# Kernel tuning notes

Hardware: AMD Instinct MI355X
Metric: run time of the kernel (lower is better)

## Reference

```python
import jax, jax.numpy as jnp
import numpy as np

B, Q, HID = 2, 1024, 2048
NH, NKV, HD = 32, 8, 64          # num heads, kv heads, head_dim (HID = NH*HD)
GROUPS = NH // NKV
KB_N, TOPK = 512, 100            # kb entries, top_k_kb
KB_MAX_TRAIN = 512               # kb_max_train_triples (kb_length_scaling=True)
ROPE_THETA = 10000.0


def rotate_half(x):
    x1, x2 = jnp.split(x, 2, axis=-1)
    return jnp.concatenate([-x2, x1], axis=-1)


def setup_inputs() -> dict:
    key = jax.random.key(0)
    ks = jax.random.split(key, 10)
    sc = 1.0 / np.sqrt(HID)
    hidden_states = jax.random.normal(ks[0], (B, Q, HID), jnp.float32)
    kb_kvs = jax.random.normal(ks[1], (B, KB_N, HID), jnp.float32)
    Wq = jax.random.normal(ks[2], (HID, NH * HD), jnp.float32) * sc
    Wk = jax.random.normal(ks[3], (HID, NKV * HD), jnp.float32) * sc
    Wv = jax.random.normal(ks[4], (HID, NKV * HD), jnp.float32) * sc
    Wo = jax.random.normal(ks[5], (NH * HD, HID), jnp.float32) * sc
    Wq_new = jax.random.normal(ks[6], (HID, NH * HD), jnp.float32) * sc
    Wkb_k = jax.random.normal(ks[7], (HID, NKV * HD), jnp.float32) * sc
    Wkb_v = jax.random.normal(ks[8], (HID, NKV * HD), jnp.float32) * sc
    # RoPE tables [Q, HD]
    inv_freq = 1.0 / (ROPE_THETA ** (jnp.arange(0, HD, 2, dtype=jnp.float32) / HD))
    t = jnp.arange(Q, dtype=jnp.float32)
    freqs = t[:, None] * inv_freq[None, :]
    emb = jnp.concatenate([freqs, freqs], axis=-1)
    cos, sin = jnp.cos(emb), jnp.sin(emb)
    position_ids = jnp.broadcast_to(jnp.arange(Q), (B, Q))
    # additive causal mask [B,1,Q,Q]
    i = jnp.arange(Q)
    causal = jnp.where(i[None, :] <= i[:, None], 0.0, -1e9).astype(jnp.float32)
    attention_mask = jnp.broadcast_to(causal[None, None], (B, 1, Q, Q))
    return dict(hidden_states=hidden_states, kb_kvs=kb_kvs, Wq=Wq, Wk=Wk, Wv=Wv,
                Wo=Wo, Wq_new=Wq_new, Wkb_k=Wkb_k, Wkb_v=Wkb_v, cos=cos, sin=sin,
                attention_mask=attention_mask, position_ids=position_ids)


def attention_fwd(hidden_states, kb_kvs, Wq, Wk, Wv, Wo, Wq_new, Wkb_k, Wkb_v,
                  cos, sin, attention_mask, position_ids):
    b, q_len, _ = hidden_states.shape
    q = (hidden_states @ Wq).reshape(b, q_len, NH, HD).transpose(0, 2, 1, 3)
    k = (hidden_states @ Wk).reshape(b, q_len, NKV, HD).transpose(0, 2, 1, 3)
    v = (hidden_states @ Wv).reshape(b, q_len, NKV, HD).transpose(0, 2, 1, 3)
    # RoPE
    c = cos[position_ids][:, None]  # [b,1,q,hd]
    s = sin[position_ids][:, None]
    q = q * c + rotate_half(q) * s
    k = k * c + rotate_half(k) * s
    # repeat_kv (GQA expansion)
    k = jnp.repeat(k, GROUPS, axis=1)
    v = jnp.repeat(v, GROUPS, axis=1)
    # KB branch (layer_idx=0, kb_layer_index=0 -> slice is full hidden dim)
    kb_k = (kb_kvs @ Wkb_k).reshape(b, KB_N, NKV, HD).transpose(0, 2, 1, 3)
    kb_v = (kb_kvs @ Wkb_v).reshape(b, KB_N, NKV, HD).transpose(0, 2, 1, 3)
    kb_k = jnp.repeat(kb_k, GROUPS, axis=1)
    kb_v = jnp.repeat(kb_v, GROUPS, axis=1)
    kb_q = (hidden_states @ Wq_new).reshape(b, q_len, NH, HD).transpose(0, 2, 1, 3)
    scale = 1.0 / jnp.sqrt(jnp.float32(HD))
    aw_kb = jnp.einsum('bhqd,bhkd->bhqk', kb_q, kb_k) * scale  # [b,nh,q,KB_N]
    # top-k KB entry selection (scores summed over heads and query positions)
    sel_scores = aw_kb.sum(axis=(1, 2))                        # [b,KB_N]
    _, top_idx = jax.lax.top_k(sel_scores, TOPK)               # [b,TOPK]
    kb_v = jnp.take_along_axis(kb_v, top_idx[:, None, :, None], axis=2)
    aw_kb = jnp.take_along_axis(aw_kb, top_idx[:, None, None, :], axis=3)
    # kb length scaling: log(max_train_triples) - log(current kb len)
    aw_kb = aw_kb + (jnp.log(jnp.float32(KB_MAX_TRAIN)) - jnp.log(jnp.float32(TOPK)))
    aw_p = jnp.einsum('bhqd,bhkd->bhqk', q, k) * scale + attention_mask
    aw = jax.nn.softmax(jnp.concatenate([aw_kb, aw_p], axis=-1).astype(jnp.float32), axis=-1)
    aw = aw.astype(q.dtype)
    cv = jnp.concatenate([kb_v, v], axis=2)                    # [b,nh,TOPK+q,hd]
    out = jnp.einsum('bhqk,bhkd->bhqd', aw, cv)
    out = out.transpose(0, 2, 1, 3).reshape(b, q_len, NH * HD)
    return out @ Wo


def reference(hidden_states, kb_kvs, Wq, Wk, Wv, Wo, Wq_new, Wkb_k, Wkb_v,
              cos, sin, attention_mask, position_ids):
    return attention_fwd(hidden_states, kb_kvs, Wq, Wk, Wv, Wo, Wq_new, Wkb_k,
                         Wkb_v, cos, sin, attention_mask, position_ids)
```

## Files before the change

### kernel.cpp

```cpp
#include <hip/hip_runtime.h>

typedef unsigned short u16;
typedef unsigned int   u32;
typedef __bf16 bf16_t;
typedef bf16_t bf16x8 __attribute__((ext_vector_type(8)));
typedef float  floatx4 __attribute__((ext_vector_type(4)));

#define B_    2
#define QS    1024
#define HID_  2048
#define NH_   32
#define NKV_  8
#define HD_   64
#define KBN_  512
#define TOPK_ 100
#define FS    5120

__device__ __forceinline__ float b2f(u16 u) {
  union { u32 i; float f; } x; x.i = ((u32)u) << 16; return x.f;
}
__device__ __forceinline__ u16 f2b(float f) {
  union { float f; u32 i; } x; x.f = f;
  u32 r = x.i + 0x7fffu + ((x.i >> 16) & 1u);
  return (u16)(r >> 16);
}
__device__ __forceinline__ void async16(const u16* g, u16* l) {
  __builtin_amdgcn_global_load_lds(
      (const __attribute__((address_space(1))) unsigned int*)g,
      (__attribute__((address_space(3))) unsigned int*)l, 16, 0, 0);
}

__global__ __launch_bounds__(256)
void tc7_k(const float* __restrict__ Wq, const float* __restrict__ Wk,
           const float* __restrict__ Wv, const float* __restrict__ Wqn,
           const float* __restrict__ Wkbk, const float* __restrict__ Wkbv,
           const float* __restrict__ Wo, u16* __restrict__ WT,
           u16* __restrict__ WTkb, u16* __restrict__ WTo,
           const float* __restrict__ hs, const float* __restrict__ kb,
           u16* __restrict__ hsb, u16* __restrict__ kbb) {
  int id = blockIdx.x, t = threadIdx.x;
  if (id >= 16384) {
    const float* x; u16* y; int j;
    if (id < 20480) { x = hs; y = hsb; j = (id - 16384) * 256 + t; }
    else            { x = kb; y = kbb; j = (id - 20480) * 256 + t; }
    float4 v = ((const float4*)x)[j];
    ((uint2*)y)[j] = make_uint2((u32)f2b(v.x) | ((u32)f2b(v.y) << 16),
                                (u32)f2b(v.z) | ((u32)f2b(v.w) << 16));
    return;
  }
  const float* W; u16* D; int N, bx, by;
  if (id < 4096)       { W = Wq;   D = WT;                        N = 2048; int l = id;         bx = l & 63; by = l >> 6; }
  else if (id < 5120)  { W = Wk;   D = WT + (size_t)2048 * 2048;  N = 512;  int l = id - 4096;  bx = l & 15; by = l >> 4; }
  else if (id < 6144)  { W = Wv;   D = WT + (size_t)2560 * 2048;  N = 512;  int l = id - 5120;  bx = l & 15; by = l >> 4; }
  else if (id < 10240) { W = Wqn;  D = WT + (size_t)3072 * 2048;  N = 2048; int l = id - 6144;  bx = l & 63; by = l >> 6; }
  else if (id < 11264) { W = Wkbk; D = WTkb;                      N = 512;  int l = id - 10240; bx = l & 15; by = l >> 4; }
  else if (id < 12288) { W = Wkbv; D = WTkb + (size_t)512 * 2048; N = 512;  int l = id - 11264; bx = l & 15; by = l >> 4; }
  else                 { W = Wo;   D = WTo;                       N = 2048; int l = id - 12288; bx = l & 63; by = l >> 6; }
  const int K = 2048;
  __shared__ float tile[32][33];
  int n0 = bx * 32, k0 = by * 32;
  int tx = t & 31, ty = t >> 5;
#pragma unroll
  for (int i = 0; i < 32; i += 8)
    tile[ty + i][tx] = W[(size_t)(k0 + ty + i) * N + n0 + tx];
  __syncthreads();
#pragma unroll
  for (int i = 0; i < 32; i += 8)
    D[(size_t)(n0 + ty + i) * K + k0 + tx] = f2b(tile[tx][ty + i]);
}

__global__ __launch_bounds__(512, 2)
void gemm256j(const u16* __restrict__ A0, const u16* __restrict__ B0,
              u16* __restrict__ C0, const u16* __restrict__ A1,
              const u16* __restrict__ B1, u16* __restrict__ C1, int K) {
  __shared__ __align__(16) u16 sm[65536];
  const int tid = threadIdx.x, lane = tid & 63, w = tid >> 6;
  const int wr = w >> 2, wc = w & 3;
  int orig = blockIdx.x;
  int swz = (orig & 7) * 22 + (orig >> 3);
  const u16 *A, *BT; u16* C; int CS, bx, by;
  if (swz < 160) { A = A0; BT = B0; C = C0; CS = FS;   bx = swz % 20; by = swz / 20; }
  else { int t2 = swz - 160; A = A1; BT = B1; C = C1; CS = 1024; bx = t2 & 3; by = t2 >> 2; }
  int m0 = by << 8, n0 = bx << 8;
  const int NT = K >> 6;

  int lr = lane >> 2;
  int colsw = ((lane & 3) * 8) ^ ((lane & 32) ? 16 : 0);
  const u16* gA[2][2]; const u16* gB[2][2];
  int lA[2][2];
#pragma unroll
  for (int h = 0; h < 2; ++h)
#pragma unroll
    for (int j = 0; j < 2; ++j) {
      int ij = 2 * w + j, kk = ij >> 3, rb = (ij & 7) * 16;
      gA[h][j] = A + (size_t)(m0 + h * 128 + rb + lr) * K + kk * 32 + colsw;
      gB[h][j] = BT + (size_t)(n0 + h * 128 + rb + lr) * K + kk * 32 + colsw;
      lA[h][j] = kk * 8192 + (h * 128 + rb) * 32;
    }
  int fsw = ((lane >> 4) * 8) ^ ((lane & 8) ? 16 : 0);
  int aoff = (wr * 128 + (lane & 15)) * 32 + fsw;
  int boff = 16384 + (wc * 64 + (lane & 15)) * 32 + fsw;

  floatx4 acc[8][4];
#pragma unroll
  for (int i = 0; i < 8; ++i)
#pragma unroll
    for (int j = 0; j < 4; ++j) acc[i][j] = (floatx4){0.f, 0.f, 0.f, 0.f};
  bf16x8 a[4][2], b[4][2];

#define STG_(g, l, u) async16((g) + (size_t)(u) * 64, &sm[(((u) & 1) << 15) + (l)])
#define BAR_ do { asm volatile("" ::: "memory"); __builtin_amdgcn_s_barrier(); \
                  asm volatile("" ::: "memory"); } while (0)
#define LG0_ do { asm volatile("s_waitcnt lgkmcnt(0)" ::: "memory"); \
                  __builtin_amdgcn_sched_barrier(0); } while (0)

  STG_(gA[0][0], lA[0][0], 0); STG_(gA[0][1], lA[0][1], 0);
  STG_(gA[1][0], lA[1][0], 0); STG_(gA[1][1], lA[1][1], 0);
  STG_(gB[0][0], lA[0][0] + 16384, 0); STG_(gB[0][1], lA[0][1] + 16384, 0);
  STG_(gB[1][0], lA[1][0] + 16384, 0); STG_(gB[1][1], lA[1][1] + 16384, 0);
  if (NT > 1) {
    STG_(gB[0][0], lA[0][0] + 16384, 1); STG_(gB[0][1], lA[0][1] + 16384, 1);
    STG_(gA[0][0], lA[0][0], 1); STG_(gA[0][1], lA[0][1], 1);
    asm volatile("s_waitcnt vmcnt(4)" ::: "memory");
  } else {
    asm volatile("s_waitcnt vmcnt(0)" ::: "memory");
  }
  BAR_;

  for (int u = 0; u < NT; ++u) {
    const int cb = (u & 1) << 15;
#pragma unroll
    for (int kk = 0; kk < 2; ++kk) {
#pragma unroll
      for (int mi = 0; mi < 4; ++mi)
        a[mi][kk] = *(const bf16x8*)&sm[cb + kk * 8192 + aoff + mi * 512];
#pragma unroll
      for (int ni = 0; ni < 2; ++ni)
        b[ni][kk] = *(const bf16x8*)&sm[cb + kk * 8192 + boff + ni * 512];
    }
    if (u + 1 < NT) { STG_(gA[1][0], lA[1][0], u + 1); STG_(gA[1][1], lA[1][1], u + 1); }
    BAR_; LG0_;
    __builtin_amdgcn_s_setprio(1);
#pragma unroll
    for (int mi = 0; mi < 4; ++mi)
#pragma unroll
      for (int ni = 0; ni < 2; ++ni)
#pragma unroll
        for (int kk = 0; kk < 2; ++kk)
          acc[mi][ni] = __builtin_amdgcn_mfma_f32_16x16x32_bf16(
              a[mi][kk], b[ni][kk], acc[mi][ni], 0, 0, 0);
    __builtin_amdgcn_s_setprio(0);
    BAR_;
#pragma unroll
    for (int kk = 0; kk < 2; ++kk)
#pragma unroll
      for (int ni = 0; ni < 2; ++ni)
        b[2 + ni][kk] = *(const bf16x8*)&sm[cb + kk * 8192 + boff + (2 + ni) * 512];
    if (u + 1 < NT) { STG_(gB[1][0], lA[1][0] + 16384, u + 1);
                      STG_(gB[1][1], lA[1][1] + 16384, u + 1); }
    BAR_; LG0_;
    __builtin_amdgcn_s_setprio(1);
#pragma unroll
    for (int mi = 0; mi < 4; ++mi)
#pragma unroll
      for (int ni = 0; ni < 2; ++ni)
#pragma unroll
        for (int kk = 0; kk < 2; ++kk)
          acc[mi][2 + ni] = __builtin_amdgcn_mfma_f32_16x16x32_bf16(
              a[mi][kk], b[2 + ni][kk], acc[mi][2 + ni], 0, 0, 0);
    __builtin_amdgcn_s_setprio(0);
    BAR_;
#pragma unroll
    for (int kk = 0; kk < 2; ++kk)
#pragma unroll
      for (int mi = 0; mi < 4; ++mi)
        a[mi][kk] = *(const bf16x8*)&sm[cb + kk * 8192 + aoff + 2048 + mi * 512];
    if (u + 2 < NT) { STG_(gB[0][0], lA[0][0] + 16384, u + 2);
                      STG_(gB[0][1], lA[0][1] + 16384, u + 2); }
    BAR_; LG0_;
    __builtin_amdgcn_s_setprio(1);
#pragma unroll
    for (int mi = 0; mi < 4; ++mi)
#pragma unroll
      for (int ni = 0; ni < 2; ++ni)
#pragma unroll
        for (int kk = 0; kk < 2; ++kk)
          acc[4 + mi][2 + ni] = __builtin_amdgcn_mfma_f32_16x16x32_bf16(
              a[mi][kk], b[2 + ni][kk], acc[4 + mi][2 + ni], 0, 0, 0);
    __builtin_amdgcn_s_setprio(0);
    BAR_;
    if (u + 2 < NT) {
      STG_(gA[0][0], lA[0][0], u + 2); STG_(gA[0][1], lA[0][1], u + 2);
      asm volatile("s_waitcnt vmcnt(4)" ::: "memory");
    } else {
      asm volatile("s_waitcnt vmcnt(0)" ::: "memory");
    }
    BAR_;
    __builtin_amdgcn_s_setprio(1);
#pragma unroll
    for (int mi = 0; mi < 4; ++mi)
#pragma unroll
      for (int ni = 0; ni < 2; ++ni)
#pragma unroll
        for (int kk = 0; kk < 2; ++kk)
          acc[4 + mi][ni] = __builtin_amdgcn_mfma_f32_16x16x32_bf16(
              a[mi][kk], b[ni][kk], acc[4 + mi][ni], 0, 0, 0);
    __builtin_amdgcn_s_setprio(0);
    BAR_;
  }
#undef STG_
#undef BAR_
#undef LG0_
  int quad = lane >> 4, col = lane & 15;
#pragma unroll
  for (int mi = 0; mi < 8; ++mi)
#pragma unroll
    for (int ni = 0; ni < 4; ++ni)
#pragma unroll
      for (int rr = 0; rr < 4; ++rr)
        C[(size_t)(m0 + wr * 128 + mi * 16 + quad * 4 + rr) * CS +
          n0 + wc * 64 + ni * 16 + col] = f2b(acc[mi][ni][rr]);
}

__global__ __launch_bounds__(512, 2)
void gemm256s(const u16* __restrict__ A, const u16* __restrict__ BT,
              float* __restrict__ P, int N, int LDK, int Kl, int ntiles) {
  __shared__ __align__(16) u16 sm[65536];
  const int tid = threadIdx.x, lane = tid & 63, w = tid >> 6;
  const int wr = w >> 2, wc = w & 3;
  const int nbx = N >> 8;
  int nwg = gridDim.x, orig = blockIdx.x, swz = orig;
  if ((nwg & 7) == 0) swz = (orig & 7) * (nwg >> 3) + (orig >> 3);
  int tile = swz % ntiles, slice = swz / ntiles;
  int bx = tile % nbx, by = tile / nbx;
  int m0 = by << 8, n0 = bx << 8;
  const int NT = Kl >> 6;
  const u16* As = A + (size_t)slice * Kl;
  const u16* Bs = BT + (size_t)slice * Kl;

  int lr = lane >> 2;
  int colsw = ((lane & 3) * 8) ^ ((lane & 32) ? 16 : 0);
  const u16* gA[2][2]; const u16* gB[2][2];
  int lA[2][2];
#pragma unroll
  for (int h = 0; h < 2; ++h)
#pragma unroll
    for (int j = 0; j < 2; ++j) {
      int ij = 2 * w + j, kk = ij >> 3, rb = (ij & 7) * 16;
      gA[h][j] = As + (size_t)(m0 + h * 128 + rb + lr) * LDK + kk * 32 + colsw;
      gB[h][j] = Bs + (size_t)(n0 + h * 128 + rb + lr) * LDK + kk * 32 + colsw;
      lA[h][j] = kk * 8192 + (h * 128 + rb) * 32;
    }
  int fsw = ((lane >> 4) * 8) ^ ((lane & 8) ? 16 : 0);
  int aoff = (wr * 128 + (lane & 15)) * 32 + fsw;
  int boff = 16384 + (wc * 64 + (lane & 15)) * 32 + fsw;

  floatx4 acc[8][4];
#pragma unroll
  for (int i = 0; i < 8; ++i)
#pragma unroll
    for (int j = 0; j < 4; ++j) acc[i][j] = (floatx4){0.f, 0.f, 0.f, 0.f};
  bf16x8 a[4][2], b[4][2];

#define STG_(g, l, u) async16((g) + (size_t)(u) * 64, &sm[(((u) & 1) << 15) + (l)])
#define BAR_ do { asm volatile("" ::: "memory"); __builtin_amdgcn_s_barrier(); \
                  asm volatile("" ::: "memory"); } while (0)
#define LG0_ do { asm volatile("s_waitcnt lgkmcnt(0)" ::: "memory"); \
                  __builtin_amdgcn_sched_barrier(0); } while (0)

  STG_(gA[0][0], lA[0][0], 0); STG_(gA[0][1], lA[0][1], 0);
  STG_(gA[1][0], lA[1][0], 0); STG_(gA[1][1], lA[1][1], 0);
  STG_(gB[0][0], lA[0][0] + 16384, 0); STG_(gB[0][1], lA[0][1] + 16384, 0);
  STG_(gB[1][0], lA[1][0] + 16384, 0); STG_(gB[1][1], lA[1][1] + 16384, 0);
  if (NT > 1) {
    STG_(gB[0][0], lA[0][0] + 16384, 1); STG_(gB[0][1], lA[0][1] + 16384, 1);
    STG_(gA[0][0], lA[0][0], 1); STG_(gA[0][1], lA[0][1], 1);
    asm volatile("s_waitcnt vmcnt(4)" ::: "memory");
  } else {
    asm volatile("s_waitcnt vmcnt(0)" ::: "memory");
  }
  BAR_;

  for (int u = 0; u < NT; ++u) {
    const int cb = (u & 1) << 15;
#pragma unroll
    for (int kk = 0; kk < 2; ++kk) {
#pragma unroll
      for (int mi = 0; mi < 4; ++mi)
        a[mi][kk] = *(const bf16x8*)&sm[cb + kk * 8192 + aoff + mi * 512];
#pragma unroll
      for (int ni = 0; ni < 2; ++ni)
        b[ni][kk] = *(const bf16x8*)&sm[cb + kk * 8192 + boff + ni * 512];
    }
    if (u + 1 < NT) { STG_(gA[1][0], lA[1][0], u + 1); STG_(gA[1][1], lA[1][1], u + 1); }
    BAR_; LG0_;
    __builtin_amdgcn_s_setprio(1);
#pragma unroll
    for (int mi = 0; mi < 4; ++mi)
#pragma unroll
      for (int ni = 0; ni < 2; ++ni)
#pragma unroll
        for (int kk = 0; kk < 2; ++kk)
          acc[mi][ni] = __builtin_amdgcn_mfma_f32_16x16x32_bf16(
              a[mi][kk], b[ni][kk], acc[mi][ni], 0, 0, 0);
    __builtin_amdgcn_s_setprio(0);
    BAR_;
#pragma unroll
    for (int kk = 0; kk < 2; ++kk)
#pragma unroll
      for (int ni = 0; ni < 2; ++ni)
        b[2 + ni][kk] = *(const bf16x8*)&sm[cb + kk * 8192 + boff + (2 + ni) * 512];
    if (u + 1 < NT) { STG_(gB[1][0], lA[1][0] + 16384, u + 1);
                      STG_(gB[1][1], lA[1][1] + 16384, u + 1); }
    BAR_; LG0_;
    __builtin_amdgcn_s_setprio(1);
#pragma unroll
    for (int mi = 0; mi < 4; ++mi)
#pragma unroll
      for (int ni = 0; ni < 2; ++ni)
#pragma unroll
        for (int kk = 0; kk < 2; ++kk)
          acc[mi][2 + ni] = __builtin_amdgcn_mfma_f32_16x16x32_bf16(
              a[mi][kk], b[2 + ni][kk], acc[mi][2 + ni], 0, 0, 0);
    __builtin_amdgcn_s_setprio(0);
    BAR_;
#pragma unroll
    for (int kk = 0; kk < 2; ++kk)
#pragma unroll
      for (int mi = 0; mi < 4; ++mi)
        a[mi][kk] = *(const bf16x8*)&sm[cb + kk * 8192 + aoff + 2048 + mi * 512];
    if (u + 2 < NT) { STG_(gB[0][0], lA[0][0] + 16384, u + 2);
                      STG_(gB[0][1], lA[0][1] + 16384, u + 2); }
    BAR_; LG0_;
    __builtin_amdgcn_s_setprio(1);
#pragma unroll
    for (int mi = 0; mi < 4; ++mi)
#pragma unroll
      for (int ni = 0; ni < 2; ++ni)
#pragma unroll
        for (int kk = 0; kk < 2; ++kk)
          acc[4 + mi][2 + ni] = __builtin_amdgcn_mfma_f32_16x16x32_bf16(
              a[mi][kk], b[2 + ni][kk], acc[4 + mi][2 + ni], 0, 0, 0);
    __builtin_amdgcn_s_setprio(0);
    BAR_;
    if (u + 2 < NT) {
      STG_(gA[0][0], lA[0][0], u + 2); STG_(gA[0][1], lA[0][1], u + 2);
      asm volatile("s_waitcnt vmcnt(4)" ::: "memory");
    } else {
      asm volatile("s_waitcnt vmcnt(0)" ::: "memory");
    }
    BAR_;
    __builtin_amdgcn_s_setprio(1);
#pragma unroll
    for (int mi = 0; mi < 4; ++mi)
#pragma unroll
      for (int ni = 0; ni < 2; ++ni)
#pragma unroll
        for (int kk = 0; kk < 2; ++kk)
          acc[4 + mi][ni] = __builtin_amdgcn_mfma_f32_16x16x32_bf16(
              a[mi][kk], b[ni][kk], acc[4 + mi][ni], 0, 0, 0);
    __builtin_amdgcn_s_setprio(0);
    BAR_;
  }
#undef STG_
#undef BAR_
#undef LG0_
  int quad = lane >> 4, col = lane & 15;
  float* Pp = P + (size_t)slice * ((size_t)ntiles << 16);
#pragma unroll
  for (int mi = 0; mi < 8; ++mi)
#pragma unroll
    for (int ni = 0; ni < 4; ++ni)
#pragma unroll
      for (int rr = 0; rr < 4; ++rr)
        Pp[(size_t)(m0 + wr * 128 + mi * 16 + quad * 4 + rr) * N +
           n0 + wc * 64 + ni * 16 + col] = acc[mi][ni][rr];
}

__global__ __launch_bounds__(256)
void redp_k(const float* __restrict__ P, float* __restrict__ out, int nslice, int len4) {
  int i = blockIdx.x * 256 + threadIdx.x;
  if (i >= len4) return;
  float4 a = ((const float4*)P)[i];
  for (int s = 1; s < nslice; ++s) {
    float4 b = ((const float4*)P)[(size_t)s * len4 + i];
    a.x += b.x; a.y += b.y; a.z += b.z; a.w += b.w;
  }
  ((float4*)out)[i] = a;
}

__global__ __launch_bounds__(256)
void rv_k(u16* __restrict__ fused, const float* __restrict__ ct,
          const float* __restrict__ st, const int* __restrict__ pid,
          u16* __restrict__ vt) {
  int bid = blockIdx.x, t = threadIdx.x;
  if (bid < 10240) {
    int gid = bid * 256 + t;
    const int nq = B_ * QS * NH_ * 32;
    u16* x; int nh, g2;
    if (gid < nq) { x = fused;        nh = NH_;  g2 = gid; }
    else          { x = fused + 2048; nh = NKV_; g2 = gid - nq; }
    int per_row = nh * 32;
    int row = g2 / per_row;
    int rem = g2 - row * per_row;
    int h = rem >> 5, d = rem & 31;
    int pos = pid[row];
    float c = ct[pos * 64 + d];
    float s = st[pos * 64 + d];
    size_t base = (size_t)row * FS + h * 64 + d;
    float x0 = b2f(x[base]), x1 = b2f(x[base + 32]);
    x[base]      = f2b(x0 * c - x1 * s);
    x[base + 32] = f2b(x1 * c + x0 * s);
    return;
  }
  int l = bid - 10240;
  int kt = l & 15, bg = l >> 4;
  int b = bg >> 3, g = bg & 7;
  __shared__ u16 tile[64][72];
  {
    int kk = t >> 2, dc = (t & 3) * 16;
    const u16* src = fused + (size_t)(b * QS + kt * 64 + kk) * FS + 2560 + g * 64 + dc;
    *(uint4*)&tile[kk][dc]     = *(const uint4*)src;
    *(uint4*)&tile[kk][dc + 8] = *(const uint4*)(src + 8);
  }
  __syncthreads();
  {
    int d = t >> 2, kc = t & 3;
    __align__(16) u16 tmp[16];
#pragma unroll
    for (int i = 0; i < 16; ++i) tmp[i] = tile[kc * 16 + i][d];
    u16* dst = vt + ((size_t)bg * 64 + d) * 1024 + kt * 64 + kc * 16;
    *(uint4*)dst       = *(uint4*)&tmp[0];
    *(uint4*)(dst + 8) = *(uint4*)&tmp[8];
  }
}

__global__ __launch_bounds__(256)
void hssum_part_k(const float* __restrict__ hs, double* __restrict__ part) {
  int qc = blockIdx.x, b = blockIdx.y, t = threadIdx.x;
  double a[8] = {0, 0, 0, 0, 0, 0, 0, 0};
  for (int qq = 0; qq < 16; ++qq) {
    const float* row = hs + (size_t)(b * QS + qc * 16 + qq) * HID_;
#pragma unroll
    for (int m = 0; m < 8; ++m) a[m] += (double)row[m * 256 + t];
  }
#pragma unroll
  for (int m = 0; m < 8; ++m)
    part[(size_t)qc * (B_ * HID_) + b * HID_ + m * 256 + t] = a[m];
}

__global__ __launch_bounds__(512)
void selS2_k(const double* __restrict__ partH, const float* __restrict__ Wqn,
             double* __restrict__ part) {
  int chunk = blockIdx.x, b = blockIdx.y, j = threadIdx.x;
  int g = j >> 6, d = j & 63;
  int c0 = chunk * 16;
  __shared__ double tmp[64][16];
  __shared__ double hsl[16];
  {
    int e = j;
    int ch = e >> 4, cc = e & 15;
    tmp[ch][cc]      = partH[(size_t)ch * (B_ * HID_) + b * HID_ + c0 + cc];
    tmp[ch + 32][cc] = partH[(size_t)(ch + 32) * (B_ * HID_) + b * HID_ + c0 + cc];
  }
  __syncthreads();
  if (j < 16) {
    double a = 0.0;
    for (int ch = 0; ch < 64; ++ch) a += tmp[ch][j];
    hsl[j] = a;
  }
  __syncthreads();
  double acc = 0.0;
  for (int cc = 0; cc < 16; ++cc) {
    int c = c0 + cc;
    const float* w = Wqn + (size_t)c * HID_ + g * 256 + d;
    acc += hsl[cc] *
           ((double)w[0] + (double)w[64] + (double)w[128] + (double)w[192]);
  }
  part[(size_t)chunk * (B_ * 512) + b * 512 + j] = acc;
}

__global__ __launch_bounds__(256)
void selU2_k(const double* __restrict__ partS, const float* __restrict__ Wkbk,
             double* __restrict__ part) {
  int jc = blockIdx.x;
  int b = blockIdx.y >> 3;
  int c = (blockIdx.y & 7) * 256 + threadIdx.x;
  int t = threadIdx.x;
  __shared__ double buf[32][128];
  __shared__ double Sl[128];
  double a = 0.0;
  if (t < 128) { }
  for (int pass = 0; pass < 4; ++pass) {
    int chb = pass * 32;
#pragma unroll
    for (int e = t; e < 4096; e += 256) {
      int ch = e >> 7, jj = e & 127;
      buf[ch][jj] = partS[(size_t)(chb + ch) * (B_ * 512) + b * 512 + jc * 128 + jj];
    }
    __syncthreads();
    if (t < 128) {
      for (int ch = 0; ch < 32; ++ch) a += buf[ch][t];
    }
    __syncthreads();
  }
  if (t < 128) Sl[t] = a;
  __syncthreads();
  const float* row = Wkbk + (size_t)c * 512 + jc * 128;
  double acc = 0.0;
  for (int j = 0; j < 128; j += 4) {
    float4 wv = *(const float4*)(row + j);
    acc += Sl[j] * (double)wv.x + Sl[j + 1] * (double)wv.y +
           Sl[j + 2] * (double)wv.z + Sl[j + 3] * (double)wv.w;
  }
  part[(size_t)jc * (B_ * HID_) + b * HID_ + c] = acc;
}

__global__ __launch_bounds__(256)
void self2_k(const double* __restrict__ partU, const float* __restrict__ kbin,
             double* __restrict__ part) {
  int n = blockIdx.x * 256 + threadIdx.x;
  int cc = blockIdx.y, b = blockIdx.z;
  int t = threadIdx.x;
  __shared__ double ul[256];
  {
    size_t ui = (size_t)b * HID_ + cc * 256 + t;
    double a = partU[ui];
    a += partU[(size_t)(B_ * HID_) + ui];
    a += partU[2 * (size_t)(B_ * HID_) + ui];
    a += partU[3 * (size_t)(B_ * HID_) + ui];
    ul[t] = a;
  }
  __syncthreads();
  const float* row = kbin + (size_t)(b * KBN_ + n) * HID_ + cc * 256;
  double acc = 0.0;
  for (int c = 0; c < 256; c += 4) {
    float4 kv = *(const float4*)(row + c);
    acc += ul[c] * (double)kv.x + ul[c + 1] * (double)kv.y +
           ul[c + 2] * (double)kv.z + ul[c + 3] * (double)kv.w;
  }
  part[(size_t)cc * (B_ * KBN_) + b * KBN_ + n] = acc;
}

__global__ __launch_bounds__(512)
void topk_rank_k(const double* __restrict__ partSel, int* __restrict__ idx) {
  int b = blockIdx.x, i = threadIdx.x;
  __shared__ float v[KBN_];
  double a = 0.0;
#pragma unroll
  for (int c = 0; c < 8; ++c) a += partSel[(size_t)c * (B_ * KBN_) + b * KBN_ + i];
  float vi = (float)a;
  v[i] = vi;
  __syncthreads();
  int rank = 0;
#pragma unroll 8
  for (int j = 0; j < KBN_; ++j) {
    float vj = v[j];
    rank += (vj > vi || (vj == vi && j < i)) ? 1 : 0;
  }
  if (rank < TOPK_) idx[b * TOPK_ + rank] = i;
}

__global__ __launch_bounds__(256)
void kbgather_k(const u16* __restrict__ kbf, const int* __restrict__ topidx,
                u16* __restrict__ kbt) {
  int bg = blockIdx.x; int b = bg >> 3, g = bg & 7;
  int t = threadIdx.x;
  int d = t >> 2, s0 = (t & 3) * 32;
  __align__(16) u16 tmp[32];
#pragma unroll
  for (int i = 0; i < 32; ++i) {
    int slot = s0 + i;
    int n = topidx[b * TOPK_ + (slot < TOPK_ ? slot : TOPK_ - 1)];
    tmp[i] = kbf[(size_t)(b * KBN_ + n) * 1024 + 512 + g * 64 + d];
  }
  u16* dst = kbt + ((size_t)bg * 64 + d) * 128 + s0;
#pragma unroll
  for (int i = 0; i < 32; i += 8) *(uint4*)(dst + i) = *(uint4*)&tmp[i];
}

__global__ __launch_bounds__(256)
void attn_mfma_k(const u16* __restrict__ fused, const u16* __restrict__ kbf,
                 const u16* __restrict__ vt, const u16* __restrict__ kbt,
                 const int* __restrict__ topidx, u16* __restrict__ ctx) {
  int bid = blockIdx.x;
  int raw = bid >> 6;
  int hb = bid & 63;
  int h = hb & 31, b = hb >> 5;
  int pg = raw >> 2, pp = raw & 3;
  int pbase = (pg >> 1) * 4 + pp;
  int qt = (pg & 1) ? (15 - pbase) : pbase;
  int g = h >> 2;
  int t = threadIdx.x, lane = t & 63, w = t >> 6;
  int quad = lane >> 4, col = lane & 15;
  __shared__ __align__(16) u16 ks[64 * 72];
  __shared__ __align__(16) u16 vst[64 * 64];
  __shared__ __align__(16) u16 ps[4][16 * 72];
  const float LOGADJ = 1.6331544f;
  int q0 = qt * 64;

  int qrow_frag = q0 + w * 16 + col;
  bf16x8 aKB[2], aC[2];
#pragma unroll
  for (int kstep = 0; kstep < 2; ++kstep) {
    const u16* p1 = fused + (size_t)(b * QS + qrow_frag) * FS + 3072 + h * 64 + kstep * 32 + quad * 8;
    const u16* p2 = fused + (size_t)(b * QS + qrow_frag) * FS + 0    + h * 64 + kstep * 32 + quad * 8;
    uint4 x1 = *(const uint4*)p1, x2 = *(const uint4*)p2;
    const u16* u1 = (const u16*)&x1; const u16* u2 = (const u16*)&x2;
#pragma unroll
    for (int i = 0; i < 8; ++i) {
      aKB[kstep][i] = (bf16_t)(0.125f * b2f(u1[i]));
      aC[kstep][i]  = (bf16_t)(0.125f * b2f(u2[i]));
    }
  }

  float mrow[4] = {-1e30f, -1e30f, -1e30f, -1e30f};
  float lrow[4] = {0.f, 0.f, 0.f, 0.f};
  floatx4 acc[4];
#pragma unroll
  for (int nb = 0; nb < 4; ++nb) acc[nb] = (floatx4){0.f, 0.f, 0.f, 0.f};

  int sj = t >> 2, sdc = (t & 3) * 16, sc4 = t & 3;
  uint4 kr0, kr1, vr0, vr1;

#define LOADTILE(TT) do {                                                      \
    int _t = (TT);                                                             \
    const u16 *_src, *_vsrc;                                                   \
    if (_t < 2) {                                                              \
      int _slot = _t * 64 + sj;                                                \
      int _n = topidx[b * TOPK_ + (_slot < TOPK_ ? _slot : TOPK_ - 1)];        \
      _src = kbf + (size_t)(b * KBN_ + _n) * 1024 + g * 64 + sdc;              \
      _vsrc = kbt + ((size_t)(b * 8 + g) * 64 + sj) * 128 + _t * 64 + sc4 * 16;\
    } else {                                                                   \
      int _key = (_t - 2) * 64 + sj;                                           \
      _src = fused + (size_t)(b * QS + _key) * FS + 2048 + g * 64 + sdc;       \
      _vsrc = vt + ((size_t)(b * 8 + g) * 64 + sj) * 1024 + (_t - 2) * 64 + sc4 * 16; \
    }                                                                          \
    kr0 = *(const uint4*)_src;  kr1 = *(const uint4*)(_src + 8);               \
    vr0 = *(const uint4*)_vsrc; vr1 = *(const uint4*)(_vsrc + 8);              \
  } while (0)

  int ntiles = 2 + (q0 >> 6) + 1;
  LOADTILE(0);
  for (int tile = 0; tile < ntiles; ++tile) {
    __syncthreads();
    *(uint4*)&ks[sj * 72 + sdc]     = kr0;
    *(uint4*)&ks[sj * 72 + sdc + 8] = kr1;
    {
      int sw = sj & 7;
      *(uint4*)&vst[sj * 64 + ((2 * sc4)     ^ sw) * 8] = vr0;
      *(uint4*)&vst[sj * 64 + ((2 * sc4 + 1) ^ sw) * 8] = vr1;
    }
    if (tile + 1 < ntiles) LOADTILE(tile + 1);
    __syncthreads();

    bf16x8 aq0 = (tile < 2) ? aKB[0] : aC[0];
    bf16x8 aq1 = (tile < 2) ? aKB[1] : aC[1];
    floatx4 s[4];
#pragma unroll
    for (int nb = 0; nb < 4; ++nb) {
      s[nb] = (floatx4){0.f, 0.f, 0.f, 0.f};
      bf16x8 b0 = *(bf16x8*)&ks[(nb * 16 + col) * 72 + quad * 8];
      bf16x8 b1 = *(bf16x8*)&ks[(nb * 16 + col) * 72 + 32 + quad * 8];
      s[nb] = __builtin_amdgcn_mfma_f32_16x16x32_bf16(aq0, b0, s[nb], 0, 0, 0);
      s[nb] = __builtin_amdgcn_mfma_f32_16x16x32_bf16(aq1, b1, s[nb], 0, 0, 0);
    }
    if (tile < 2) {
      if (tile == 0) {
#pragma unroll
        for (int nb = 0; nb < 4; ++nb)
#pragma unroll
          for (int rr = 0; rr < 4; ++rr) s[nb][rr] += LOGADJ;
      } else {
#pragma unroll
        for (int nb = 0; nb < 4; ++nb) {
          bool dead = (64 + nb * 16 + col) >= TOPK_;
#pragma unroll
          for (int rr = 0; rr < 4; ++rr)
            s[nb][rr] = dead ? -1e30f : (s[nb][rr] + LOGADJ);
        }
      }
    } else if (tile == ntiles - 1) {
      int kbase = (tile - 2) * 64;
#pragma unroll
      for (int nb = 0; nb < 4; ++nb) {
        int key = kbase + nb * 16 + col;
#pragma unroll
        for (int rr = 0; rr < 4; ++rr) {
          int qrow = q0 + w * 16 + quad * 4 + rr;
          if (key > qrow) s[nb][rr] = -1e30f;
        }
      }
    }
    float tm[4];
#pragma unroll
    for (int rr = 0; rr < 4; ++rr)
      tm[rr] = fmaxf(fmaxf(s[0][rr], s[1][rr]), fmaxf(s[2][rr], s[3][rr]));
#pragma unroll
    for (int off = 1; off < 16; off <<= 1)
#pragma unroll
      for (int rr = 0; rr < 4; ++rr)
        tm[rr] = fmaxf(tm[rr], __shfl_xor(tm[rr], off));
    float alpha[4], rs[4];
#pragma unroll
    for (int rr = 0; rr < 4; ++rr) {
      float mn = fmaxf(mrow[rr], tm[rr]);
      alpha[rr] = __expf(mrow[rr] - mn);
      mrow[rr] = mn;
      rs[rr] = 0.f;
    }
#pragma unroll
    for (int nb = 0; nb < 4; ++nb)
#pragma unroll
      for (int rr = 0; rr < 4; ++rr) {
        float ev = __expf(s[nb][rr] - mrow[rr]);
        rs[rr] += ev;
        ps[w][(quad * 4 + rr) * 72 + nb * 16 + col] = f2b(ev);
      }
#pragma unroll
    for (int off = 1; off < 16; off <<= 1)
#pragma unroll
      for (int rr = 0; rr < 4; ++rr)
        rs[rr] += __shfl_xor(rs[rr], off);
#pragma unroll
    for (int rr = 0; rr < 4; ++rr) lrow[rr] = lrow[rr] * alpha[rr] + rs[rr];
#pragma unroll
    for (int nb = 0; nb < 4; ++nb)
#pragma unroll
      for (int rr = 0; rr < 4; ++rr) acc[nb][rr] *= alpha[rr];

    bf16x8 pa0 = *(bf16x8*)&ps[w][col * 72 + quad * 8];
    bf16x8 pa1 = *(bf16x8*)&ps[w][col * 72 + 32 + quad * 8];
#pragma unroll
    for (int nb = 0; nb < 4; ++nb) {
      int d = nb * 16 + col;
      int sw = (d & 7) << 3;
      bf16x8 vb0 = *(bf16x8*)&vst[d * 64 + ((quad * 8) ^ sw)];
      bf16x8 vb1 = *(bf16x8*)&vst[d * 64 + ((32 + quad * 8) ^ sw)];
      acc[nb] = __builtin_amdgcn_mfma_f32_16x16x32_bf16(pa0, vb0, acc[nb], 0, 0, 0);
      acc[nb] = __builtin_amdgcn_mfma_f32_16x16x32_bf16(pa1, vb1, acc[nb], 0, 0, 0);
    }
  }
#undef LOADTILE
#pragma unroll
  for (int rr = 0; rr < 4; ++rr) {
    float inv = 1.f / lrow[rr];
    int qrow = q0 + w * 16 + quad * 4 + rr;
    size_t base = (size_t)(b * QS + qrow) * HID_ + h * 64;
#pragma unroll
    for (int nb = 0; nb < 4; ++nb)
      ctx[base + nb * 16 + col] = f2b(acc[nb][rr] * inv);
  }
}

extern "C" void kernel_launch(void* const* d_in, const int* in_sizes, int n_in,
                              void* d_out, int out_size, void* d_ws, size_t ws_size,
                              hipStream_t stream) {
  (void)in_sizes; (void)n_in; (void)out_size; (void)ws_size;
  const float* hs_f = (const float*)d_in[0];
  const float* kb_f = (const float*)d_in[1];
  const float* Wq   = (const float*)d_in[2];
  const float* Wk   = (const float*)d_in[3];
  const float* Wv   = (const float*)d_in[4];
  const float* Wo   = (const float*)d_in[5];
  const float* Wqn  = (const float*)d_in[6];
  const float* Wkbk = (const float*)d_in[7];
  const float* Wkbv = (const float*)d_in[8];
  const float* cosT = (const float*)d_in[9];
  const float* sinT = (const float*)d_in[10];
  const int*   pid  = (const int*)d_in[12];
  float* out = (float*)d_out;

  char* p = (char*)d_ws;
  u16* WT    = (u16*)p; p += (size_t)FS * 2048 * 2;
  u16* WTkb  = (u16*)p; p += (size_t)1024 * 2048 * 2;
  u16* WTo   = (u16*)p; p += (size_t)2048 * 2048 * 2;
  u16* fused = (u16*)p; p += (size_t)B_ * QS * FS * 2;
  u16* hs_b  = (u16*)p; p += (size_t)B_ * QS * HID_ * 2;
  u16* kb_b  = (u16*)p; p += (size_t)B_ * KBN_ * HID_ * 2;
  u16* kbf   = (u16*)p; p += (size_t)B_ * KBN_ * 1024 * 2;
  int*    idx_ws   = (int*)p;    p += (size_t)B_ * TOPK_ * 4 + 4;
  double* partH    = (double*)p; p += (size_t)64 * B_ * HID_ * 8;
  double* partS    = (double*)p; p += (size_t)128 * B_ * 512 * 8;
  double* partU    = (double*)p; p += (size_t)4 * B_ * HID_ * 8;
  double* partSel  = (double*)p; p += (size_t)8 * B_ * KBN_ * 8;
  float*  partKG   = (float*)p;  p += (size_t)4 * 2048 * 2048 * 4;
  u16* ctx_ws = hs_b;
  u16* v_t    = kb_b;
  u16* kb_t   = kb_b + (size_t)B_ * 8 * 64 * 1024;

  dim3 blk(256);
  tc7_k<<<dim3(22528), blk, 0, stream>>>(Wq, Wk, Wv, Wqn, Wkbk, Wkbv, Wo,
                                         WT, WTkb, WTo, hs_f, kb_f, hs_b, kb_b);
  gemm256j<<<dim3(176), dim3(512), 0, stream>>>(hs_b, WT, fused, kb_b, WTkb, kbf, 2048);
  rv_k<<<dim3(10496), blk, 0, stream>>>(fused, cosT, sinT, pid, v_t);
  hssum_part_k<<<dim3(64, B_), blk, 0, stream>>>(hs_f, partH);
  selS2_k<<<dim3(128, B_), dim3(512), 0, stream>>>(partH, Wqn, partS);
  selU2_k<<<dim3(4, B_ * 8), blk, 0, stream>>>(partS, Wkbk, partU);
  self2_k<<<dim3(2, 8, B_), blk, 0, stream>>>(partU, kb_f, partSel);
  topk_rank_k<<<dim3(B_), dim3(512), 0, stream>>>(partSel, idx_ws);
  kbgather_k<<<dim3(B_ * 8), blk, 0, stream>>>(kbf, idx_ws, kb_t);
  attn_mfma_k<<<dim3(16 * NH_ * B_), blk, 0, stream>>>(fused, kbf, v_t, kb_t, idx_ws, ctx_ws);
  gemm256s<<<dim3(64 * 4), dim3(512), 0, stream>>>(ctx_ws, WTo, partKG, 2048, 2048, 512, 64);
  redp_k<<<dim3((2048 * 2048 / 4 + 255) / 256), blk, 0, stream>>>(
      partKG, out, 4, 2048 * 2048 / 4);
}
```

Before: 368.4 us.

## Fold selection-score kernels into existing launches and use atomic split-K output

The hs-sum, selS and selU kernels become extra blocks appended to the transpose, projection GEMM and RoPE/V-transpose kernels, which removes three launches and lets that small work run alongside the big kernels. The split-K output GEMM now adds its slices straight into a zeroed output with float atomics instead of writing a 64MB partial buffer and running a separate reduction kernel. In exchange it adds a memset, atomic contention on every output element, and a summation order that is no longer deterministic. The side-work blocks also share the GEMM's large shared-memory allocation, which can affect occupancy for those blocks.

```diff
diff --git a/kernel.cpp b/kernel.cpp
--- a/kernel.cpp
+++ b/kernel.cpp
@@ -37,8 +37,23 @@
            const float* __restrict__ Wo, u16* __restrict__ WT,
            u16* __restrict__ WTkb, u16* __restrict__ WTo,
            const float* __restrict__ hs, const float* __restrict__ kb,
-           u16* __restrict__ hsb, u16* __restrict__ kbb) {
+           u16* __restrict__ hsb, u16* __restrict__ kbb,
+           double* __restrict__ partH) {
   int id = blockIdx.x, t = threadIdx.x;
+  if (id >= 22528) {
+    int l = id - 22528;
+    int qc = l & 63, b = l >> 6;
+    double a[8] = {0, 0, 0, 0, 0, 0, 0, 0};
+    for (int qq = 0; qq < 16; ++qq) {
+      const float* row = hs + (size_t)(b * QS + qc * 16 + qq) * HID_;
+#pragma unroll
+      for (int m = 0; m < 8; ++m) a[m] += (double)row[m * 256 + t];
+    }
+#pragma unroll
+    for (int m = 0; m < 8; ++m)
+      partH[(size_t)qc * (B_ * HID_) + b * HID_ + m * 256 + t] = a[m];
+    return;
+  }
   if (id >= 16384) {
     const float* x; u16* y; int j;
     if (id < 20480) { x = hs; y = hsb; j = (id - 16384) * 256 + t; }
@@ -72,11 +87,42 @@
 __global__ __launch_bounds__(512, 2)
 void gemm256j(const u16* __restrict__ A0, const u16* __restrict__ B0,
               u16* __restrict__ C0, const u16* __restrict__ A1,
-              const u16* __restrict__ B1, u16* __restrict__ C1, int K) {
+              const u16* __restrict__ B1, u16* __restrict__ C1, int K,
+              const double* __restrict__ partH, const float* __restrict__ Wqn,
+              double* __restrict__ partS) {
   __shared__ __align__(16) u16 sm[65536];
   const int tid = threadIdx.x, lane = tid & 63, w = tid >> 6;
+  int orig = blockIdx.x;
+  if (orig >= 176) {
+    int l = orig - 176;
+    int chunk = l & 127, b = l >> 7, j = tid;
+    double* tmpd = (double*)sm;
+    double* hsl  = tmpd + 1024;
+    int g = j >> 6, d = j & 63;
+    int c0 = chunk * 16;
+    {
+      int ch = j >> 4, cc = j & 15;
+      tmpd[ch * 16 + cc]        = partH[(size_t)ch * (B_ * HID_) + b * HID_ + c0 + cc];
+      tmpd[(ch + 32) * 16 + cc] = partH[(size_t)(ch + 32) * (B_ * HID_) + b * HID_ + c0 + cc];
+    }
+    __syncthreads();
+    if (j < 16) {
+      double a = 0.0;
+      for (int ch = 0; ch < 64; ++ch) a += tmpd[ch * 16 + j];
+      hsl[j] = a;
+    }
+    __syncthreads();
+    double acc = 0.0;
+    for (int cc = 0; cc < 16; ++cc) {
+      int c = c0 + cc;
+      const float* wq = Wqn + (size_t)c * HID_ + g * 256 + d;
+      acc += hsl[cc] *
+             ((double)wq[0] + (double)wq[64] + (double)wq[128] + (double)wq[192]);
+    }
+    partS[(size_t)chunk * (B_ * 512) + b * 512 + j] = acc;
+    return;
+  }
   const int wr = w >> 2, wc = w & 3;
-  int orig = blockIdx.x;
   int swz = (orig & 7) * 22 + (orig >> 3);
   const u16 *A, *BT; u16* C; int CS, bx, by;
   if (swz < 160) { A = A0; BT = B0; C = C0; CS = FS;   bx = swz % 20; by = swz / 20; }
@@ -224,7 +270,7 @@
 
 __global__ __launch_bounds__(512, 2)
 void gemm256s(const u16* __restrict__ A, const u16* __restrict__ BT,
-              float* __restrict__ P, int N, int LDK, int Kl, int ntiles) {
+              float* __restrict__ Out, int N, int LDK, int Kl, int ntiles) {
   __shared__ __align__(16) u16 sm[65536];
   const int tid = threadIdx.x, lane = tid & 63, w = tid >> 6;
   const int wr = w >> 2, wc = w & 3;
@@ -366,33 +412,22 @@
 #undef BAR_
 #undef LG0_
   int quad = lane >> 4, col = lane & 15;
-  float* Pp = P + (size_t)slice * ((size_t)ntiles << 16);
 #pragma unroll
   for (int mi = 0; mi < 8; ++mi)
 #pragma unroll
     for (int ni = 0; ni < 4; ++ni)
 #pragma unroll
       for (int rr = 0; rr < 4; ++rr)
-        Pp[(size_t)(m0 + wr * 128 + mi * 16 + quad * 4 + rr) * N +
-           n0 + wc * 64 + ni * 16 + col] = acc[mi][ni][rr];
-}
-
-__global__ __launch_bounds__(256)
-void redp_k(const float* __restrict__ P, float* __restrict__ out, int nslice, int len4) {
-  int i = blockIdx.x * 256 + threadIdx.x;
-  if (i >= len4) return;
-  float4 a = ((const float4*)P)[i];
-  for (int s = 1; s < nslice; ++s) {
-    float4 b = ((const float4*)P)[(size_t)s * len4 + i];
-    a.x += b.x; a.y += b.y; a.z += b.z; a.w += b.w;
-  }
-  ((float4*)out)[i] = a;
+        unsafeAtomicAdd(&Out[(size_t)(m0 + wr * 128 + mi * 16 + quad * 4 + rr) * N +
+                             n0 + wc * 64 + ni * 16 + col], acc[mi][ni][rr]);
 }
 
 __global__ __launch_bounds__(256)
 void rv_k(u16* __restrict__ fused, const float* __restrict__ ct,
           const float* __restrict__ st, const int* __restrict__ pid,
-          u16* __restrict__ vt) {
+          u16* __restrict__ vt, const double* __restrict__ partS,
+          const float* __restrict__ Wkbk, double* __restrict__ partU) {
+  __shared__ __align__(16) char rsm[33792];
   int bid = blockIdx.x, t = threadIdx.x;
   if (bid < 10240) {
     int gid = bid * 256 + t;
@@ -413,107 +448,59 @@
     x[base + 32] = f2b(x1 * c + x0 * s);
     return;
   }
+  if (bid >= 10496) {
+    int l = bid - 10496;
+    int jc = l & 3, yy = l >> 2;
+    int b = yy >> 3;
+    int c = (yy & 7) * 256 + t;
+    double* buf = (double*)rsm;
+    double* Sl  = (double*)(rsm + 32768);
+    double a = 0.0;
+    for (int pass = 0; pass < 4; ++pass) {
+      int chb = pass * 32;
+#pragma unroll
+      for (int e = t; e < 4096; e += 256) {
+        int ch = e >> 7, jj = e & 127;
+        buf[ch * 128 + jj] = partS[(size_t)(chb + ch) * (B_ * 512) + b * 512 + jc * 128 + jj];
+      }
+      __syncthreads();
+      if (t < 128) {
+        for (int ch = 0; ch < 32; ++ch) a += buf[ch * 128 + t];
+      }
+      __syncthreads();
+    }
+    if (t < 128) Sl[t] = a;
+    __syncthreads();
+    const float* row = Wkbk + (size_t)c * 512 + jc * 128;
+    double acc = 0.0;
+    for (int j = 0; j < 128; j += 4) {
+      float4 wv = *(const float4*)(row + j);
+      acc += Sl[j] * (double)wv.x + Sl[j + 1] * (double)wv.y +
+             Sl[j + 2] * (double)wv.z + Sl[j + 3] * (double)wv.w;
+    }
+    partU[(size_t)jc * (B_ * HID_) + b * HID_ + c] = acc;
+    return;
+  }
   int l = bid - 10240;
   int kt = l & 15, bg = l >> 4;
   int b = bg >> 3, g = bg & 7;
-  __shared__ u16 tile[64][72];
+  u16* tile = (u16*)rsm;
   {
     int kk = t >> 2, dc = (t & 3) * 16;
     const u16* src = fused + (size_t)(b * QS + kt * 64 + kk) * FS + 2560 + g * 64 + dc;
-    *(uint4*)&tile[kk][dc]     = *(const uint4*)src;
-    *(uint4*)&tile[kk][dc + 8] = *(const uint4*)(src + 8);
+    *(uint4*)&tile[kk * 72 + dc]     = *(const uint4*)src;
+    *(uint4*)&tile[kk * 72 + dc + 8] = *(const uint4*)(src + 8);
   }
   __syncthreads();
   {
     int d = t >> 2, kc = t & 3;
     __align__(16) u16 tmp[16];
 #pragma unroll
-    for (int i = 0; i < 16; ++i) tmp[i] = tile[kc * 16 + i][d];
+    for (int i = 0; i < 16; ++i) tmp[i] = tile[(kc * 16 + i) * 72 + d];
     u16* dst = vt + ((size_t)bg * 64 + d) * 1024 + kt * 64 + kc * 16;
     *(uint4*)dst       = *(uint4*)&tmp[0];
     *(uint4*)(dst + 8) = *(uint4*)&tmp[8];
   }
-}
-
-__global__ __launch_bounds__(256)
-void hssum_part_k(const float* __restrict__ hs, double* __restrict__ part) {
-  int qc = blockIdx.x, b = blockIdx.y, t = threadIdx.x;
-  double a[8] = {0, 0, 0, 0, 0, 0, 0, 0};
-  for (int qq = 0; qq < 16; ++qq) {
-    const float* row = hs + (size_t)(b * QS + qc * 16 + qq) * HID_;
-#pragma unroll
-    for (int m = 0; m < 8; ++m) a[m] += (double)row[m * 256 + t];
-  }
-#pragma unroll
-  for (int m = 0; m < 8; ++m)
-    part[(size_t)qc * (B_ * HID_) + b * HID_ + m * 256 + t] = a[m];
-}
-
-__global__ __launch_bounds__(512)
-void selS2_k(const double* __restrict__ partH, const float* __restrict__ Wqn,
-             double* __restrict__ part) {
-  int chunk = blockIdx.x, b = blockIdx.y, j = threadIdx.x;
-  int g = j >> 6, d = j & 63;
-  int c0 = chunk * 16;
-  __shared__ double tmp[64][16];
-  __shared__ double hsl[16];
-  {
-    int e = j;
-    int ch = e >> 4, cc = e & 15;
-    tmp[ch][cc]      = partH[(size_t)ch * (B_ * HID_) + b * HID_ + c0 + cc];
-    tmp[ch + 32][cc] = partH[(size_t)(ch + 32) * (B_ * HID_) + b * HID_ + c0 + cc];
-  }
-  __syncthreads();
-  if (j < 16) {
-    double a = 0.0;
-    for (int ch = 0; ch < 64; ++ch) a += tmp[ch][j];
-    hsl[j] = a;
-  }
-  __syncthreads();
-  double acc = 0.0;
-  for (int cc = 0; cc < 16; ++cc) {
-    int c = c0 + cc;
-    const float* w = Wqn + (size_t)c * HID_ + g * 256 + d;
-    acc += hsl[cc] *
-           ((double)w[0] + (double)w[64] + (double)w[128] + (double)w[192]);
-  }
-  part[(size_t)chunk * (B_ * 512) + b * 512 + j] = acc;
-}
-
-__global__ __launch_bounds__(256)
-void selU2_k(const double* __restrict__ partS, const float* __restrict__ Wkbk,
-             double* __restrict__ part) {
-  int jc = blockIdx.x;
-  int b = blockIdx.y >> 3;
-  int c = (blockIdx.y & 7) * 256 + threadIdx.x;
-  int t = threadIdx.x;
-  __shared__ double buf[32][128];
-  __shared__ double Sl[128];
-  double a = 0.0;
-  if (t < 128) { }
-  for (int pass = 0; pass < 4; ++pass) {
-    int chb = pass * 32;
-#pragma unroll
-    for (int e = t; e < 4096; e += 256) {
-      int ch = e >> 7, jj = e & 127;
-      buf[ch][jj] = partS[(size_t)(chb + ch) * (B_ * 512) + b * 512 + jc * 128 + jj];
-    }
-    __syncthreads();
-    if (t < 128) {
-      for (int ch = 0; ch < 32; ++ch) a += buf[ch][t];
-    }
-    __syncthreads();
-  }
-  if (t < 128) Sl[t] = a;
-  __syncthreads();
-  const float* row = Wkbk + (size_t)c * 512 + jc * 128;
-  double acc = 0.0;
-  for (int j = 0; j < 128; j += 4) {
-    float4 wv = *(const float4*)(row + j);
-    acc += Sl[j] * (double)wv.x + Sl[j + 1] * (double)wv.y +
-           Sl[j + 2] * (double)wv.z + Sl[j + 3] * (double)wv.w;
-  }
-  part[(size_t)jc * (B_ * HID_) + b * HID_ + c] = acc;
 }
 
 __global__ __launch_bounds__(256)
@@ -784,24 +771,21 @@
   double* partS    = (double*)p; p += (size_t)128 * B_ * 512 * 8;
   double* partU    = (double*)p; p += (size_t)4 * B_ * HID_ * 8;
   double* partSel  = (double*)p; p += (size_t)8 * B_ * KBN_ * 8;
-  float*  partKG   = (float*)p;  p += (size_t)4 * 2048 * 2048 * 4;
   u16* ctx_ws = hs_b;
   u16* v_t    = kb_b;
   u16* kb_t   = kb_b + (size_t)B_ * 8 * 64 * 1024;
 
   dim3 blk(256);
-  tc7_k<<<dim3(22528), blk, 0, stream>>>(Wq, Wk, Wv, Wqn, Wkbk, Wkbv, Wo,
-                                         WT, WTkb, WTo, hs_f, kb_f, hs_b, kb_b);
-  gemm256j<<<dim3(176), dim3(512), 0, stream>>>(hs_b, WT, fused, kb_b, WTkb, kbf, 2048);
-  rv_k<<<dim3(10496), blk, 0, stream>>>(fused, cosT, sinT, pid, v_t);
-  hssum_part_k<<<dim3(64, B_), blk, 0, stream>>>(hs_f, partH);
-  selS2_k<<<dim3(128, B_), dim3(512), 0, stream>>>(partH, Wqn, partS);
-  selU2_k<<<dim3(4, B_ * 8), blk, 0, stream>>>(partS, Wkbk, partU);
+  hipMemsetAsync(out, 0, (size_t)2048 * 2048 * 4, stream);
+  tc7_k<<<dim3(22656), blk, 0, stream>>>(Wq, Wk, Wv, Wqn, Wkbk, Wkbv, Wo,
+                                         WT, WTkb, WTo, hs_f, kb_f, hs_b, kb_b, partH);
+  gemm256j<<<dim3(432), dim3(512), 0, stream>>>(hs_b, WT, fused, kb_b, WTkb, kbf, 2048,
+                                                partH, Wqn, partS);
+  rv_k<<<dim3(10560), blk, 0, stream>>>(fused, cosT, sinT, pid, v_t,
+                                        partS, Wkbk, partU);
   self2_k<<<dim3(2, 8, B_), blk, 0, stream>>>(partU, kb_f, partSel);
   topk_rank_k<<<dim3(B_), dim3(512), 0, stream>>>(partSel, idx_ws);
   kbgather_k<<<dim3(B_ * 8), blk, 0, stream>>>(kbf, idx_ws, kb_t);
   attn_mfma_k<<<dim3(16 * NH_ * B_), blk, 0, stream>>>(fused, kbf, v_t, kb_t, idx_ws, ctx_ws);
-  gemm256s<<<dim3(64 * 4), dim3(512), 0, stream>>>(ctx_ws, WTo, partKG, 2048, 2048, 512, 64);
-  redp_k<<<dim3((2048 * 2048 / 4 + 255) / 256), blk, 0, stream>>>(
-      partKG, out, 4, 2048 * 2048 / 4);
-}
+  gemm256s<<<dim3(64 * 4), dim3(512), 0, stream>>>(ctx_ws, WTo, out, 2048, 2048, 512, 64);
+}
```

After: 393.7 us. 1.07x slower.
